# Performance work log

Hardware: AMD Instinct MI355X
Metric: run time of the kernel (lower is better)

The kernel has to match this reference:

```python
import jax, jax.numpy as jnp
import numpy as np

SEQ_LEN = 4096
EMBED_DIM = 2048
NUM_HEADS = 16
HEAD_DIM = EMBED_DIM // NUM_HEADS


def setup_inputs() -> dict:
    key = jax.random.key(0)
    k1, k2, k3 = jax.random.split(key, 3)
    x = jax.random.normal(k1, (SEQ_LEN, EMBED_DIM), dtype=jnp.float32)
    # Dense-layer params (lecun-normal-ish scaling for stability)
    W_qkv = jax.random.normal(k2, (EMBED_DIM, 3 * EMBED_DIM), dtype=jnp.float32) / np.sqrt(EMBED_DIM)
    b_qkv = jnp.zeros((3 * EMBED_DIM,), dtype=jnp.float32)
    W_out = jax.random.normal(k3, (EMBED_DIM, EMBED_DIM), dtype=jnp.float32) / np.sqrt(EMBED_DIM)
    b_out = jnp.zeros((EMBED_DIM,), dtype=jnp.float32)
    return {"x": x, "W_qkv": W_qkv, "b_qkv": b_qkv, "W_out": W_out, "b_out": b_out}


def reference(x, W_qkv, b_qkv, W_out, b_out):
    seq_len = x.shape[0]
    qkv = x @ W_qkv + b_qkv                       # (S, 3E)
    qkv = qkv.reshape(seq_len, 3, NUM_HEADS, HEAD_DIM)
    q, k, v = qkv[:, 0], qkv[:, 1], qkv[:, 2]     # each (S, H, D)
    scale = 1.0 / jnp.sqrt(jnp.float32(HEAD_DIM))
    # NOTE: faithful to source -- contracts over BOTH heads and head_dim,
    # producing a single (S, S) attention matrix shared across heads.
    attn = jnp.einsum('thd,shd->ts', q, k) * scale
    causal = jnp.triu(jnp.ones((seq_len, seq_len), dtype=bool), k=1)
    attn = jnp.where(causal, -jnp.inf, attn)
    attn = jax.nn.softmax(attn, axis=-1)
    out = jnp.einsum('ts,shd->thd', attn, v)      # (S, H, D)
    out = out.reshape(seq_len, EMBED_DIM)
    return out @ W_out + b_out
```

## Files before the change

### kernel.cpp

```cpp
#include <hip/hip_runtime.h>
#include <cstdint>
#include <cstddef>

#define SEQLEN 4096
#define EMBED  2048
#define NH     16
#define HD     128
#define N3     6144
#define SCALE  0.08838834764831845f
#define MBIAS  25.0f
#define LB3    12288

typedef __attribute__((ext_vector_type(8))) short bf16x8;
typedef __attribute__((ext_vector_type(4))) float f32x4;
typedef unsigned short u16;

#define MFMA(a, b, c) __builtin_amdgcn_mfma_f32_16x16x32_bf16((a), (b), (c), 0, 0, 0)

__device__ inline u16 f2bf(float f) {
  uint32_t u = __float_as_uint(f);
  u += 0x7FFF + ((u >> 16) & 1);
  return (u16)(u >> 16);
}

__device__ inline float bf2f(u16 u) {
  return __uint_as_float(((uint32_t)u) << 16);
}

__device__ inline void gload_lds16(const u16* g, u16* l) {
  __builtin_amdgcn_global_load_lds((const __attribute__((address_space(1))) void*)g,
                                   (__attribute__((address_space(3))) void*)l, 16, 0, 0);
}

__device__ __forceinline__ void stage3(const u16* a0, const u16* a1, const u16* b0,
                                       u16* base, int w, int lane) {
  gload_lds16(a0, base + w * 512 + lane * 8);
  gload_lds16(a1, base + 4096 + w * 512 + lane * 8);
  gload_lds16(b0, base + 8192 + w * 512 + lane * 8);
}

__device__ __forceinline__ void mm256x128(const u16* gA, size_t sA, const u16* gB, size_t sB,
                                          int NT, u16* lds, f32x4 (&acc)[4][4]) {
  int tid = threadIdx.x;
  int w = tid >> 6, lane = tid & 63;
  int g = lane >> 4, lr = lane & 15;
  int wm = w >> 1, wn = w & 1;
  int arow = (w << 4) + (lane >> 2);
  int cb = (((lane & 3) ^ (arow & 3)) << 3);
  const u16* a0 = gA + (size_t)arow * sA + cb;
  const u16* a1 = gA + (size_t)(128 + arow) * sA + cb;
  const u16* b0 = gB + (size_t)arow * sB + cb;
  int gx = ((g ^ (lr & 3)) << 3);
  int aoff = ((wm << 6) + lr) * 32 + gx;
  int boff = 8192 + ((wn << 6) + lr) * 32 + gx;
  stage3(a0, a1, b0, lds, w, lane);
  stage3(a0 + 32, a1 + 32, b0 + 32, lds + LB3, w, lane);
  asm volatile("s_waitcnt vmcnt(3)" ::: "memory");
  __builtin_amdgcn_s_barrier();
  for (int t = 0; t < NT; ++t) {
    u16* base = lds + (t % 3) * LB3;
    bf16x8 af[4], bfr[4];
    #pragma unroll
    for (int m = 0; m < 4; m++) af[m] = *(const bf16x8*)(base + aoff + m * 512);
    #pragma unroll
    for (int n = 0; n < 4; n++) bfr[n] = *(const bf16x8*)(base + boff + n * 512);
    if (t + 2 < NT) {
      int kt = (t + 2) << 5;
      stage3(a0 + kt, a1 + kt, b0 + kt, lds + ((t + 2) % 3) * LB3, w, lane);
    }
    __builtin_amdgcn_s_setprio(1);
    #pragma unroll
    for (int m = 0; m < 4; m++)
      #pragma unroll
      for (int n = 0; n < 4; n++)
        acc[m][n] = MFMA(af[m], bfr[n], acc[m][n]);
    __builtin_amdgcn_s_setprio(0);
    if (t + 1 < NT) {
      if (t + 2 < NT) asm volatile("s_waitcnt vmcnt(3)" ::: "memory");
      else            asm volatile("s_waitcnt vmcnt(0)" ::: "memory");
      __builtin_amdgcn_s_barrier();
    }
  }
  asm volatile("" ::: "memory");
}

__global__ __launch_bounds__(256) void conv_f32_bf16(const float* __restrict__ in,
                                                     u16* __restrict__ out, int n) {
  int i = (blockIdx.x * 256 + threadIdx.x) * 4;
  if (i >= n) return;
  float4 v = *(const float4*)(in + i);
  ushort4 o;
  o.x = f2bf(v.x); o.y = f2bf(v.y); o.z = f2bf(v.z); o.w = f2bf(v.w);
  *(ushort4*)(out + i) = o;
}

__global__ __launch_bounds__(256) void transpose_conv(const float* __restrict__ in,
                                                      u16* __restrict__ out, int R, int C) {
  __shared__ float t[32][33];
  int c0 = blockIdx.x * 32, r0 = blockIdx.y * 32;
  int tx = threadIdx.x, ty = threadIdx.y;
  #pragma unroll
  for (int i = ty; i < 32; i += 8)
    t[i][tx] = in[(size_t)(r0 + i) * C + c0 + tx];
  __syncthreads();
  #pragma unroll
  for (int i = ty; i < 32; i += 8)
    out[(size_t)(c0 + i) * R + r0 + tx] = f2bf(t[tx][i]);
}

__global__ __launch_bounds__(256) void vtrans(const u16* __restrict__ qkv, u16* __restrict__ vT) {
  __shared__ u16 t[32][33];
  int c0 = blockIdx.x * 32, t0 = blockIdx.y * 32;
  int tx = threadIdx.x, ty = threadIdx.y;
  #pragma unroll
  for (int i = ty; i < 32; i += 8)
    t[i][tx] = qkv[(size_t)(t0 + i) * N3 + 2 * EMBED + c0 + tx];
  __syncthreads();
  #pragma unroll
  for (int i = ty; i < 32; i += 8)
    vT[(size_t)(c0 + i) * SEQLEN + t0 + tx] = t[tx][i];
}

__global__ __launch_bounds__(512, 4) void gemm_bt2(const u16* __restrict__ A, const u16* __restrict__ Bt,
                                                   const float* __restrict__ bias,
                                                   u16* __restrict__ Cb, float* __restrict__ Cf,
                                                   int M, int N, int K, int out_f32) {
  __shared__ __align__(16) u16 lds[3 * LB3];
  int bn = blockIdx.x, bm = blockIdx.y;
  f32x4 acc[4][4] = {};
  mm256x128(A + (size_t)(bm * 256) * K, K, Bt + (size_t)(bn * 128) * K, K, K >> 5, lds, acc);
  int tid = threadIdx.x;
  int w = tid >> 6, lane = tid & 63, g = lane >> 4, lr = lane & 15;
  int wm = w >> 1, wn = w & 1;
  int r0 = bm * 256 + wm * 64, c0 = bn * 128 + wn * 64;
  #pragma unroll
  for (int n = 0; n < 4; n++) {
    int c = c0 + n * 16 + lr;
    float bv = bias[c];
    #pragma unroll
    for (int m = 0; m < 4; m++)
      #pragma unroll
      for (int j = 0; j < 4; j++) {
        int r = r0 + m * 16 + g * 4 + j;
        float v = acc[m][n][j] + bv;
        if (out_f32) Cf[(size_t)r * N + c] = v;
        else         Cb[(size_t)r * N + c] = f2bf(v);
      }
  }
}

__global__ __launch_bounds__(512, 4) void sgemm_p2(const u16* __restrict__ qkv,
                                                   u16* __restrict__ P) {
  int bx = blockIdx.x, by = blockIdx.y;
  int r0g = by * 256, c0g = bx * 128;
  if (c0g > r0g + 255) return;
  __shared__ __align__(16) u16 lds[3 * LB3];
  f32x4 acc[4][4] = {};
  mm256x128(qkv + (size_t)r0g * N3, N3, qkv + (size_t)c0g * N3 + EMBED, N3, EMBED >> 5, lds, acc);
  int tid = threadIdx.x;
  int w = tid >> 6, lane = tid & 63, g = lane >> 4, lr = lane & 15;
  int wm = w >> 1, wn = w & 1;
  int r0 = r0g + wm * 64, c0 = c0g + wn * 64;
  #pragma unroll
  for (int m = 0; m < 4; m++)
    #pragma unroll
    for (int n = 0; n < 4; n++) {
      int c = c0 + n * 16 + lr;
      #pragma unroll
      for (int j = 0; j < 4; j++) {
        int r = r0 + m * 16 + g * 4 + j;
        float p = (c <= r) ? __expf(fmaf(acc[m][n][j], SCALE, -MBIAS)) : 0.f;
        P[(size_t)r * SEQLEN + c] = f2bf(p);
      }
    }
}

__global__ __launch_bounds__(256) void psum(const u16* __restrict__ P, float* __restrict__ L) {
  int wave = threadIdx.x >> 6, lane = threadIdx.x & 63;
  int r = blockIdx.x * 4 + wave;
  int ctop = ((r >> 8) + 1) * 256;
  const u16* Prow = P + (size_t)r * SEQLEN;
  float s = 0.f;
  for (int c = lane * 8; c < ctop; c += 512) {
    bf16x8 v = *(const bf16x8*)(Prow + c);
    #pragma unroll
    for (int j = 0; j < 8; j++) s += bf2f((u16)v[j]);
  }
  s += __shfl_xor(s, 1);  s += __shfl_xor(s, 2);  s += __shfl_xor(s, 4);
  s += __shfl_xor(s, 8);  s += __shfl_xor(s, 16); s += __shfl_xor(s, 32);
  if (lane == 0) L[r] = s;
}

__global__ __launch_bounds__(512, 4) void pv_gemm2(const u16* __restrict__ P,
                                                   const u16* __restrict__ vT,
                                                   const float* __restrict__ L,
                                                   u16* __restrict__ O) {
  int bx = blockIdx.x, by = blockIdx.y;
  int r0g = by * 256, c0g = bx * 128;
  int NT = (r0g + 256) >> 5;
  __shared__ __align__(16) u16 lds[3 * LB3];
  f32x4 acc[4][4] = {};
  mm256x128(P + (size_t)r0g * SEQLEN, SEQLEN, vT + (size_t)c0g * SEQLEN, SEQLEN, NT, lds, acc);
  int tid = threadIdx.x;
  int w = tid >> 6, lane = tid & 63, g = lane >> 4, lr = lane & 15;
  int wm = w >> 1, wn = w & 1;
  int r0 = r0g + wm * 64, c0 = c0g + wn * 64;
  #pragma unroll
  for (int m = 0; m < 4; m++) {
    float invl[4];
    #pragma unroll
    for (int j = 0; j < 4; j++)
      invl[j] = 1.f / L[r0 + m * 16 + g * 4 + j];
    #pragma unroll
    for (int n = 0; n < 4; n++) {
      int c = c0 + n * 16 + lr;
      #pragma unroll
      for (int j = 0; j < 4; j++) {
        int r = r0 + m * 16 + g * 4 + j;
        O[(size_t)r * EMBED + c] = f2bf(acc[m][n][j] * invl[j]);
      }
    }
  }
}

extern "C" void kernel_launch(void* const* d_in, const int* in_sizes, int n_in,
                              void* d_out, int out_size, void* d_ws, size_t ws_size,
                              hipStream_t stream) {
  const float* x     = (const float*)d_in[0];
  const float* W_qkv = (const float*)d_in[1];
  const float* b_qkv = (const float*)d_in[2];
  const float* W_out = (const float*)d_in[3];
  const float* b_out = (const float*)d_in[4];
  float* out = (float*)d_out;

  u16* xb    = (u16*)d_ws;
  u16* qkvb  = xb + (size_t)SEQLEN * EMBED;
  u16* Pbuf  = qkvb + (size_t)SEQLEN * N3;
  u16* vT    = Pbuf + (size_t)SEQLEN * SEQLEN;
  float* Lbuf = (float*)(vT + (size_t)EMBED * SEQLEN);
  u16* attb  = xb;
  u16* WqkvT = Pbuf;
  u16* WoutT = Pbuf;

  conv_f32_bf16<<<SEQLEN * EMBED / 1024, 256, 0, stream>>>(x, xb, SEQLEN * EMBED);
  transpose_conv<<<dim3(N3 / 32, EMBED / 32), dim3(32, 8), 0, stream>>>(W_qkv, WqkvT, EMBED, N3);
  gemm_bt2<<<dim3(N3 / 128, SEQLEN / 256), 512, 0, stream>>>(xb, WqkvT, b_qkv, qkvb, nullptr,
                                                             SEQLEN, N3, EMBED, 0);
  vtrans<<<dim3(EMBED / 32, SEQLEN / 32), dim3(32, 8), 0, stream>>>(qkvb, vT);
  sgemm_p2<<<dim3(SEQLEN / 128, SEQLEN / 256), 512, 0, stream>>>(qkvb, Pbuf);
  psum<<<SEQLEN / 4, 256, 0, stream>>>(Pbuf, Lbuf);
  pv_gemm2<<<dim3(EMBED / 128, SEQLEN / 256), 512, 0, stream>>>(Pbuf, vT, Lbuf, attb);
  transpose_conv<<<dim3(EMBED / 32, EMBED / 32), dim3(32, 8), 0, stream>>>(W_out, WoutT, EMBED, EMBED);
  gemm_bt2<<<dim3(EMBED / 128, SEQLEN / 256), 512, 0, stream>>>(attb, WoutT, b_out, nullptr, out,
                                                                SEQLEN, EMBED, EMBED, 1);
}
```

Baseline: 334.8 us.

## Balance causal PV GEMM by pairing short and long 128-row tiles per block

Replaces the 256x128 PV tile kernel with a 128x128 tile kernel where each block processes two row tiles, one from the top and one from the bottom of the causal triangle, so every block does roughly the same K-loop length. This targets load imbalance from the triangular P matrix, where blocks for late rows ran far longer than early ones. Smaller tiles lower per-block arithmetic intensity and need a barrier between passes, but LDS use per block drops.

```diff
diff --git a/kernel.cpp b/kernel.cpp
--- a/kernel.cpp
+++ b/kernel.cpp
@@ -10,6 +10,7 @@
 #define SCALE  0.08838834764831845f
 #define MBIAS  25.0f
 #define LB3    12288
+#define LB1    8192
 
 typedef __attribute__((ext_vector_type(8))) short bf16x8;
 typedef __attribute__((ext_vector_type(4))) float f32x4;
@@ -48,7 +49,7 @@
   int arow = (w << 4) + (lane >> 2);
   int cb = (((lane & 3) ^ (arow & 3)) << 3);
   const u16* a0 = gA + (size_t)arow * sA + cb;
-  const u16* a1 = gA + (size_t)(128 + arow) * sA + cb;
+  const u16* a1 = a0 + (size_t)128 * sA;
   const u16* b0 = gB + (size_t)arow * sB + cb;
   int gx = ((g ^ (lr & 3)) << 3);
   int aoff = ((wm << 6) + lr) * 32 + gx;
@@ -84,6 +85,55 @@
   asm volatile("" ::: "memory");
 }
 
+__device__ __forceinline__ void stage2h(const u16* a0, const u16* b0, u16* base, int w, int lane) {
+  gload_lds16(a0, base + w * 512 + lane * 8);
+  gload_lds16(b0, base + 4096 + w * 512 + lane * 8);
+}
+
+__device__ __forceinline__ void mm128x128(const u16* gA, size_t sA, const u16* gB, size_t sB,
+                                          int NT, u16* lds, f32x4 (&acc)[4][2]) {
+  int tid = threadIdx.x;
+  int w = tid >> 6, lane = tid & 63;
+  int g = lane >> 4, lr = lane & 15;
+  int wm = w >> 2, wn = w & 3;
+  int srow = lane >> 2;
+  int cb = (((lane & 3) ^ (srow & 3)) << 3);
+  const u16* a0 = gA + (size_t)((w << 4) + srow) * sA + cb;
+  const u16* b0 = gB + (size_t)((w << 4) + srow) * sB + cb;
+  int gx = ((g ^ (lr & 3)) << 3);
+  int aoff = ((wm << 6) + lr) * 32 + gx;
+  int boff = 4096 + ((wn << 5) + lr) * 32 + gx;
+  stage2h(a0, b0, lds, w, lane);
+  stage2h(a0 + 32, b0 + 32, lds + LB1, w, lane);
+  asm volatile("s_waitcnt vmcnt(2)" ::: "memory");
+  __builtin_amdgcn_s_barrier();
+  for (int t = 0; t < NT; ++t) {
+    u16* base = lds + (t % 3) * LB1;
+    bf16x8 af[4], bfr[2];
+    #pragma unroll
+    for (int m = 0; m < 4; m++) af[m] = *(const bf16x8*)(base + aoff + m * 512);
+    #pragma unroll
+    for (int n = 0; n < 2; n++) bfr[n] = *(const bf16x8*)(base + boff + n * 512);
+    if (t + 2 < NT) {
+      int kt = (t + 2) << 5;
+      stage2h(a0 + kt, b0 + kt, lds + ((t + 2) % 3) * LB1, w, lane);
+    }
+    __builtin_amdgcn_s_setprio(1);
+    #pragma unroll
+    for (int m = 0; m < 4; m++)
+      #pragma unroll
+      for (int n = 0; n < 2; n++)
+        acc[m][n] = MFMA(af[m], bfr[n], acc[m][n]);
+    __builtin_amdgcn_s_setprio(0);
+    if (t + 1 < NT) {
+      if (t + 2 < NT) asm volatile("s_waitcnt vmcnt(2)" ::: "memory");
+      else            asm volatile("s_waitcnt vmcnt(0)" ::: "memory");
+      __builtin_amdgcn_s_barrier();
+    }
+  }
+  asm volatile("" ::: "memory");
+}
+
 __global__ __launch_bounds__(256) void conv_f32_bf16(const float* __restrict__ in,
                                                      u16* __restrict__ out, int n) {
   int i = (blockIdx.x * 256 + threadIdx.x) * 4;
@@ -191,35 +241,41 @@
   if (lane == 0) L[r] = s;
 }
 
-__global__ __launch_bounds__(512, 4) void pv_gemm2(const u16* __restrict__ P,
+__global__ __launch_bounds__(512, 4) void pv_gemm3(const u16* __restrict__ P,
                                                    const u16* __restrict__ vT,
                                                    const float* __restrict__ L,
                                                    u16* __restrict__ O) {
-  int bx = blockIdx.x, by = blockIdx.y;
-  int r0g = by * 256, c0g = bx * 128;
-  int NT = (r0g + 256) >> 5;
-  __shared__ __align__(16) u16 lds[3 * LB3];
-  f32x4 acc[4][4] = {};
-  mm256x128(P + (size_t)r0g * SEQLEN, SEQLEN, vT + (size_t)c0g * SEQLEN, SEQLEN, NT, lds, acc);
+  __shared__ __align__(16) u16 lds[3 * LB1];
+  int bx = blockIdx.x, pp = blockIdx.y;
   int tid = threadIdx.x;
   int w = tid >> 6, lane = tid & 63, g = lane >> 4, lr = lane & 15;
-  int wm = w >> 1, wn = w & 1;
-  int r0 = r0g + wm * 64, c0 = c0g + wn * 64;
-  #pragma unroll
-  for (int m = 0; m < 4; m++) {
-    float invl[4];
-    #pragma unroll
-    for (int j = 0; j < 4; j++)
-      invl[j] = 1.f / L[r0 + m * 16 + g * 4 + j];
-    #pragma unroll
-    for (int n = 0; n < 4; n++) {
-      int c = c0 + n * 16 + lr;
-      #pragma unroll
-      for (int j = 0; j < 4; j++) {
-        int r = r0 + m * 16 + g * 4 + j;
-        O[(size_t)r * EMBED + c] = f2bf(acc[m][n][j] * invl[j]);
+  int wm = w >> 2, wn = w & 3;
+  int c0g = bx * 128;
+  #pragma unroll
+  for (int pass = 0; pass < 2; pass++) {
+    int rt = pass ? pp : (31 - pp);
+    int r0g = rt * 128;
+    int NT = (r0g + 128) >> 5;
+    f32x4 acc[4][2] = {};
+    mm128x128(P + (size_t)r0g * SEQLEN, SEQLEN, vT + (size_t)c0g * SEQLEN, SEQLEN, NT, lds, acc);
+    int r0 = r0g + wm * 64, c0 = c0g + wn * 32;
+    #pragma unroll
+    for (int m = 0; m < 4; m++) {
+      float invl[4];
+      #pragma unroll
+      for (int j = 0; j < 4; j++)
+        invl[j] = 1.f / L[r0 + m * 16 + g * 4 + j];
+      #pragma unroll
+      for (int n = 0; n < 2; n++) {
+        int c = c0 + n * 16 + lr;
+        #pragma unroll
+        for (int j = 0; j < 4; j++) {
+          int r = r0 + m * 16 + g * 4 + j;
+          O[(size_t)r * EMBED + c] = f2bf(acc[m][n][j] * invl[j]);
+        }
       }
     }
+    __syncthreads();
   }
 }
 
@@ -249,7 +305,7 @@
   vtrans<<<dim3(EMBED / 32, SEQLEN / 32), dim3(32, 8), 0, stream>>>(qkvb, vT);
   sgemm_p2<<<dim3(SEQLEN / 128, SEQLEN / 256), 512, 0, stream>>>(qkvb, Pbuf);
   psum<<<SEQLEN / 4, 256, 0, stream>>>(Pbuf, Lbuf);
-  pv_gemm2<<<dim3(EMBED / 128, SEQLEN / 256), 512, 0, stream>>>(Pbuf, vT, Lbuf, attb);
+  pv_gemm3<<<dim3(EMBED / 128, 16), 512, 0, stream>>>(Pbuf, vT, Lbuf, attb);
   transpose_conv<<<dim3(EMBED / 32, EMBED / 32), dim3(32, 8), 0, stream>>>(W_out, WoutT, EMBED, EMBED);
   gemm_bt2<<<dim3(EMBED / 128, SEQLEN / 256), 512, 0, stream>>>(attb, WoutT, b_out, nullptr, out,
                                                                 SEQLEN, EMBED, EMBED, 1);
```

New measurement: 318.2 us. 4.9% less time.
